# Performance work log

Hardware: AMD Instinct MI355X
Metric: run time of the kernel (lower is better)

## Reference

```python
import jax, jax.numpy as jnp
import numpy as np

N_NODES = 100000
N_EDGES = 1600000
F_IN = 256
EMB = 16  # conv1 out = 2*EMB = 32, conv2 out = EMB


def setup_inputs() -> dict:
    key = jax.random.key(0)
    k1, k2, k3, k4, k5, k6, k7 = jax.random.split(key, 7)
    x = jax.random.normal(k1, (N_NODES, F_IN), dtype=jnp.float32)
    edge_index = jax.random.randint(k2, (2, N_EDGES), 0, N_NODES, dtype=jnp.int64)
    edge_weight = jax.random.uniform(k3, (N_EDGES,), dtype=jnp.float32)
    # GCNConv params: glorot-ish weights, zero bias (materialized as params)
    s1 = 1.0 / np.sqrt(F_IN)
    s2 = 1.0 / np.sqrt(2 * EMB)
    W1 = jax.random.uniform(k4, (F_IN, 2 * EMB), minval=-s1, maxval=s1, dtype=jnp.float32)
    b1 = jnp.zeros((2 * EMB,), dtype=jnp.float32)
    W2 = jax.random.uniform(k5, (2 * EMB, EMB), minval=-s2, maxval=s2, dtype=jnp.float32)
    b2 = jnp.zeros((EMB,), dtype=jnp.float32)
    return {"x": x, "edge_index": edge_index, "edge_weight": edge_weight,
            "W1": W1, "b1": b1, "W2": W2, "b2": b2}


def _gcn_norm(edge_index, edge_weight, num_nodes, dtype):
    # PyG gcn_norm with add_self_loops=True, fill_value=1.0
    row, col = edge_index[0], edge_index[1]
    loop = jnp.arange(num_nodes)
    row_a = jnp.concatenate([row, loop])
    col_a = jnp.concatenate([col, loop])
    w_a = jnp.concatenate([edge_weight, jnp.ones((num_nodes,), dtype=dtype)])
    deg = jax.ops.segment_sum(w_a, col_a, num_segments=num_nodes)
    dinv = jnp.where(deg > 0, jax.lax.rsqrt(deg), jnp.zeros_like(deg))
    norm = dinv[row_a] * w_a * dinv[col_a]
    return row_a, col_a, norm


def _gcn_conv(x, W, b, row, col, norm, num_nodes):
    h = x @ W                                  # [N, d_out] dense projection
    msg = norm[:, None] * h[row]               # gather + edge scale, [E+N, d_out]
    out = jax.ops.segment_sum(msg, col, num_segments=num_nodes)  # scatter-add
    return out + b


def reference(x, edge_index, edge_weight, W1, b1, W2, b2):
    n = x.shape[0]
    row, col, norm = _gcn_norm(edge_index, edge_weight, n, x.dtype)
    h = jax.nn.relu(_gcn_conv(x, W1, b1, row, col, norm, n))
    return _gcn_conv(h, W2, b2, row, col, norm, n)
```

## Files before the change

kernel.cpp:

```cpp
#include <hip/hip_runtime.h>
#include <hip/hip_bf16.h>

#define NN   100000
#define NE   1600000
#define FIN  256
#define HID  32
#define OUTD 16
#define NBLK ((NN + 255) / 256)

#define BM          64
#define GEMM_BLOCKS ((NN + BM - 1) / BM)
#define CNT_EDGES   2048
#define CNT_BLOCKS  ((NE + CNT_EDGES - 1) / CNT_EDGES)
#define FILL_BLOCKS ((NE + 1023) / 1024)

#define OFF_FLAG    0
#define OFF_DEG     64
#define OFF_DINV    (OFF_DEG + NN)
#define OFF_RANK    (OFF_DINV + NN)
#define OFF_BSUM    (OFF_RANK + NE)
#define OFF_ROWPTR  (OFF_BSUM + 1024)
#define OFF_CSR     (OFF_ROWPTR + NN + 32)
#define OFF_H1      (OFF_CSR + 2*NE)
#define OFF_P2      (OFF_H1 + NN*HID)

#define CSHIFT 26
#define CMASK  ((1u << CSHIFT) - 1u)
#define WSCALE 1048576.0f
#define WINV   (1.0f / 1048576.0f)

__device__ __forceinline__ float bf2f(unsigned short u) {
  union { unsigned int i; float f; } v; v.i = ((unsigned int)u) << 16; return v.f;
}
__device__ __forceinline__ unsigned short f2bf(float f) {
  union { float f; unsigned int i; } v; v.f = f;
  unsigned int x = v.i;
  return (unsigned short)((x + 0x7fffu + ((x >> 16) & 1u)) >> 16);
}
__device__ __forceinline__ int eidx(const int* __restrict__ ei, long long pos, int is64) {
  return is64 ? ei[2 * pos] : ei[pos];
}
__device__ __forceinline__ float ldf(const void* p, long long i, int isf32) {
  return isf32 ? ((const float*)p)[i] : bf2f(((const unsigned short*)p)[i]);
}

__global__ __launch_bounds__(256) void detect_zero_kernel(const int* __restrict__ ei,
    const unsigned short* __restrict__ xu, int* __restrict__ flags,
    unsigned int* __restrict__ zp, int zn) {
  int b = blockIdx.x;
  if (b == 0) {
    __shared__ int any, cnt;
    if (threadIdx.x == 0) { any = 0; cnt = 0; }
    __syncthreads();
    int local = 0, c = 0;
    for (int i = threadIdx.x; i < 2048; i += 256) local |= ei[2 * i + 1];
    for (int i = threadIdx.x; i < 1024; i += 256) {
      unsigned int e = (xu[2 * i] >> 7) & 0xFF;
      c += (e < 100 || e > 140) ? 1 : 0;
    }
    if (local) atomicOr(&any, 1);
    atomicAdd(&cnt, c);
    __syncthreads();
    if (threadIdx.x == 0) {
      flags[0] = (any == 0) ? 1 : 0;
      flags[1] = (cnt > 100) ? 1 : 0;
    }
  } else {
    int stride = (gridDim.x - 1) * 256;
    for (int i = (b - 1) * 256 + threadIdx.x; i < zn; i += stride) zp[i] = 0u;
  }
}

__global__ __launch_bounds__(256) void count_kernel(const int* __restrict__ ei,
    const void* __restrict__ ew, unsigned int* __restrict__ deg,
    int* __restrict__ rank, const int* __restrict__ flags) {
  int t = threadIdx.x;
  int is64 = flags[0], isf32 = flags[1];
  int e0 = blockIdx.x * CNT_EDGES + t;
  int c[8]; float w[8];
  #pragma unroll
  for (int q = 0; q < 8; q++) {
    int e = e0 + q * 256;
    if (e < NE) {
      c[q] = eidx(ei, (long long)NE + e, is64);
      w[q] = ldf(ew, e, isf32);
    } else c[q] = -1;
  }
  unsigned int old[8];
  #pragma unroll
  for (int q = 0; q < 8; q++) {
    if (c[q] >= 0) {
      unsigned int inc = (1u << CSHIFT) | (unsigned int)(w[q] * WSCALE + 0.5f);
      old[q] = atomicAdd(deg + c[q], inc);
    }
  }
  #pragma unroll
  for (int q = 0; q < 8; q++)
    if (c[q] >= 0) rank[e0 + q * 256] = (int)(old[q] >> CSHIFT);
}

__global__ __launch_bounds__(256, 8) void gemm1_kernel(const void* __restrict__ x,
    const void* __restrict__ W1, float* __restrict__ h1,
    const int* __restrict__ flags) {
  __shared__ float xs[32][BM + 2];
  __shared__ float wl[32][36];
  int b = blockIdx.x;
  int t = threadIdx.x;
  int rb = b * BM;
  int isf32 = flags[1];

  int j0 = (t & 15) * 2;
  int r0 = (t >> 4) * 4;
  int rr  = t >> 2;
  int kk0 = (t & 3) * 8;
  int kkw = t >> 3;
  int mw  = (t & 7) * 4;
  long long grow = (long long)rb + rr;

  float acc[4][2];
  #pragma unroll
  for (int i = 0; i < 4; i++) { acc[i][0] = 0.f; acc[i][1] = 0.f; }

  union Pf { uint4 u[2]; float f[8]; unsigned short s[16]; } pfx;
  uint4 pw;

#define LOADX(kc_) do {                                                        \
    if (grow < NN) {                                                           \
      if (isf32) {                                                             \
        const float* xp_ = (const float*)x + grow * FIN + (kc_) + kk0;         \
        pfx.u[0] = ((const uint4*)xp_)[0];                                     \
        pfx.u[1] = ((const uint4*)xp_)[1];                                     \
      } else {                                                                 \
        const unsigned short* xp_ = (const unsigned short*)x + grow * FIN + (kc_) + kk0; \
        pfx.u[0] = *(const uint4*)xp_;                                         \
      }                                                                        \
    }                                                                          \
  } while (0)

#define STOREX() do {                                                          \
    bool ok_ = grow < NN;                                                      \
    if (isf32) {                                                               \
      _Pragma("unroll")                                                        \
      for (int q = 0; q < 8; q++) xs[kk0 + q][rr] = ok_ ? pfx.f[q] : 0.f;      \
    } else {                                                                   \
      _Pragma("unroll")                                                        \
      for (int q = 0; q < 8; q++) xs[kk0 + q][rr] = ok_ ? bf2f(pfx.s[q]) : 0.f;\
    }                                                                          \
  } while (0)

#define LOADW(kc_) do {                                                        \
    if (isf32) {                                                               \
      pw = *(const uint4*)((const float*)W1 + ((kc_) + kkw) * HID + mw);       \
    } else {                                                                   \
      const unsigned short* wp_ = (const unsigned short*)W1 + ((kc_) + kkw) * HID + mw; \
      pw.x = ((const unsigned int*)wp_)[0];                                    \
      pw.y = ((const unsigned int*)wp_)[1];                                    \
    }                                                                          \
  } while (0)

#define STOREW() do {                                                          \
    if (isf32) {                                                               \
      *(float4*)&wl[kkw][mw] = *(float4*)&pw;                                  \
    } else {                                                                   \
      const unsigned short* ps_ = (const unsigned short*)&pw;                  \
      wl[kkw][mw + 0] = bf2f(ps_[0]); wl[kkw][mw + 1] = bf2f(ps_[1]);          \
      wl[kkw][mw + 2] = bf2f(ps_[2]); wl[kkw][mw + 3] = bf2f(ps_[3]);          \
    }                                                                          \
  } while (0)

  LOADX(0); LOADW(0);

  for (int kc = 0; kc < FIN; kc += 32) {
    __syncthreads();
    STOREX(); STOREW();
    __syncthreads();
    if (kc + 32 < FIN) { LOADX(kc + 32); LOADW(kc + 32); }
    #pragma unroll 8
    for (int kk = 0; kk < 32; kk++) {
      float2 wp2 = *(const float2*)&wl[kk][j0];
      float2 xa = *(const float2*)&xs[kk][r0];
      float2 xb = *(const float2*)&xs[kk][r0 + 2];
      float xv[4] = {xa.x, xa.y, xb.x, xb.y};
      #pragma unroll
      for (int i = 0; i < 4; i++) {
        acc[i][0] = fmaf(xv[i], wp2.x, acc[i][0]);
        acc[i][1] = fmaf(xv[i], wp2.y, acc[i][1]);
      }
    }
  }

  #pragma unroll
  for (int i = 0; i < 4; i++) {
    int g = rb + r0 + i;
    if (g < NN) {
      float2 v; v.x = acc[i][0]; v.y = acc[i][1];
      *((float2*)(h1 + (long long)g * HID + j0)) = v;
    }
  }
#undef LOADX
#undef STOREX
#undef LOADW
#undef STOREW
}

__global__ __launch_bounds__(256) void dinv_scansum_kernel(
    const unsigned int* __restrict__ deg, float* __restrict__ dinv,
    int* __restrict__ bsum) {
  int b = blockIdx.x;
  if (b < NBLK) {
    __shared__ int s[256];
    int i = b * 256 + threadIdx.x;
    s[threadIdx.x] = (i < NN) ? (int)(deg[i] >> CSHIFT) : 0;
    __syncthreads();
    for (int off = 128; off > 0; off >>= 1) {
      if (threadIdx.x < off) s[threadIdx.x] += s[threadIdx.x + off];
      __syncthreads();
    }
    if (threadIdx.x == 0) bsum[b] = s[0];
  } else {
    int i = (b - NBLK) * 256 + threadIdx.x;
    if (i >= NN) return;
    float d = (float)(deg[i] & CMASK) * WINV + 1.0f;
    dinv[i] = rsqrtf(d);
  }
}

__global__ __launch_bounds__(256) void scan_write_kernel(const unsigned int* __restrict__ deg,
    const int* __restrict__ bsum, int* __restrict__ rowptr) {
  __shared__ int a[256];
  __shared__ int base_s;
  int t = threadIdx.x;
  int b = blockIdx.x;
  int v = 0;
  for (int i = t; i < NBLK; i += 256) v += (i < b) ? bsum[i] : 0;
  a[t] = v;
  __syncthreads();
  for (int off = 128; off > 0; off >>= 1) {
    if (t < off) a[t] += a[t + off];
    __syncthreads();
  }
  if (t == 0) base_s = a[0];
  __syncthreads();
  int base = base_s;
  int i = b * 256 + t;
  int orig = (i < NN) ? (int)(deg[i] >> CSHIFT) : 0;
  a[t] = orig;
  __syncthreads();
  for (int off = 1; off < 256; off <<= 1) {
    int x2 = a[t] + ((t >= off) ? a[t - off] : 0);
    __syncthreads();
    a[t] = x2;
    __syncthreads();
  }
  if (i < NN) rowptr[i] = base + a[t] - orig;
  if (b == 0 && t == 0) rowptr[NN] = NE;
}

__global__ __launch_bounds__(256) void fill_csr_kernel(const int* __restrict__ ei,
    const void* __restrict__ ew, const float* __restrict__ dinv,
    const int* __restrict__ rowptr, const int* __restrict__ rank,
    int2* __restrict__ csr, const int* __restrict__ flags) {
  int is64 = flags[0], isf32 = flags[1];
  int e0 = blockIdx.x * 1024 + threadIdx.x;
  int r[4], c[4], rk[4]; float w[4];
  #pragma unroll
  for (int q = 0; q < 4; q++) {
    int e = e0 + q * 256;
    if (e < NE) {
      r[q]  = eidx(ei, e, is64);
      c[q]  = eidx(ei, (long long)NE + e, is64);
      w[q]  = ldf(ew, e, isf32);
      rk[q] = rank[e];
    } else c[q] = -1;
  }
  float dr[4], dc[4]; int rp[4];
  #pragma unroll
  for (int q = 0; q < 4; q++) {
    if (c[q] >= 0) {
      dr[q] = dinv[r[q]];
      dc[q] = dinv[c[q]];
      rp[q] = rowptr[c[q]];
    }
  }
  #pragma unroll
  for (int q = 0; q < 4; q++) {
    if (c[q] >= 0) {
      int2 pr; pr.x = r[q]; pr.y = __float_as_int(dr[q] * w[q] * dc[q]);
      csr[rp[q] + rk[q]] = pr;
    }
  }
}

__global__ __launch_bounds__(256) void gather1_kernel(const float* __restrict__ h1,
    const float* __restrict__ dinv, const int* __restrict__ rowptr,
    const int2* __restrict__ csr, const void* __restrict__ b1,
    const void* __restrict__ W2, float* __restrict__ p2,
    const int* __restrict__ flags) {
  __shared__ float w2lds[HID * OUTD];
  __shared__ float b1l[HID];
  __shared__ float tl[8][HID + 1];
  int t = threadIdx.x;
  int isf32 = flags[1];
  w2lds[2 * t]     = ldf(W2, 2 * t, isf32);
  w2lds[2 * t + 1] = ldf(W2, 2 * t + 1, isf32);
  if (t < HID) b1l[t] = ldf(b1, t, isf32);
  __syncthreads();

  int nl = t >> 5;
  int j  = t & 31;
  int node = blockIdx.x * 8 + nl;
  if (node < NN) {
    int k0 = rowptr[node], k1 = rowptr[node + 1];
    float acc = 0.f;
    int k = k0;
    for (; k + 8 <= k1; k += 8) {
      int2 q0 = csr[k];     int2 q1 = csr[k + 1];
      int2 q2 = csr[k + 2]; int2 q3 = csr[k + 3];
      int2 q4 = csr[k + 4]; int2 q5 = csr[k + 5];
      int2 q6 = csr[k + 6]; int2 q7 = csr[k + 7];
      float v0 = h1[q0.x * HID + j]; float v1 = h1[q1.x * HID + j];
      float v2 = h1[q2.x * HID + j]; float v3 = h1[q3.x * HID + j];
      float v4 = h1[q4.x * HID + j]; float v5 = h1[q5.x * HID + j];
      float v6 = h1[q6.x * HID + j]; float v7 = h1[q7.x * HID + j];
      acc = fmaf(__int_as_float(q0.y), v0, acc);
      acc = fmaf(__int_as_float(q1.y), v1, acc);
      acc = fmaf(__int_as_float(q2.y), v2, acc);
      acc = fmaf(__int_as_float(q3.y), v3, acc);
      acc = fmaf(__int_as_float(q4.y), v4, acc);
      acc = fmaf(__int_as_float(q5.y), v5, acc);
      acc = fmaf(__int_as_float(q6.y), v6, acc);
      acc = fmaf(__int_as_float(q7.y), v7, acc);
    }
    for (; k + 4 <= k1; k += 4) {
      int2 q0 = csr[k];     int2 q1 = csr[k + 1];
      int2 q2 = csr[k + 2]; int2 q3 = csr[k + 3];
      float v0 = h1[q0.x * HID + j]; float v1 = h1[q1.x * HID + j];
      float v2 = h1[q2.x * HID + j]; float v3 = h1[q3.x * HID + j];
      acc = fmaf(__int_as_float(q0.y), v0, acc);
      acc = fmaf(__int_as_float(q1.y), v1, acc);
      acc = fmaf(__int_as_float(q2.y), v2, acc);
      acc = fmaf(__int_as_float(q3.y), v3, acc);
    }
    for (; k < k1; k++) {
      int2 pr = csr[k];
      acc = fmaf(__int_as_float(pr.y), h1[pr.x * HID + j], acc);
    }
    float di = dinv[node];
    acc = fmaf(di * di, h1[node * HID + j], acc);
    acc += b1l[j];
    tl[nl][j] = fmaxf(acc, 0.f);
  }
  __syncthreads();
  int m = t & 31;
  if (node < NN && m < OUTD) {
    float s = 0.f;
    #pragma unroll
    for (int k = 0; k < HID; k++) s = fmaf(tl[nl][k], w2lds[k * OUTD + m], s);
    p2[node * OUTD + m] = s;
  }
}

__global__ __launch_bounds__(256) void gather2_kernel(const float* __restrict__ p2,
    const float* __restrict__ dinv, const int* __restrict__ rowptr,
    const int2* __restrict__ csr, const void* __restrict__ b2,
    void* __restrict__ out, const int* __restrict__ flags) {
  __shared__ float b2l[OUTD];
  int t = threadIdx.x;
  int isf32 = flags[1];
  if (t < OUTD) b2l[t] = ldf(b2, t, isf32);
  __syncthreads();

  int nl = t >> 4;
  int m  = t & 15;
  int node = blockIdx.x * 16 + nl;
  if (node >= NN) return;
  int k0 = rowptr[node], k1 = rowptr[node + 1];
  float acc = 0.f;
  int k = k0;
  for (; k + 8 <= k1; k += 8) {
    int2 q0 = csr[k];     int2 q1 = csr[k + 1];
    int2 q2 = csr[k + 2]; int2 q3 = csr[k + 3];
    int2 q4 = csr[k + 4]; int2 q5 = csr[k + 5];
    int2 q6 = csr[k + 6]; int2 q7 = csr[k + 7];
    float v0 = p2[q0.x * OUTD + m]; float v1 = p2[q1.x * OUTD + m];
    float v2 = p2[q2.x * OUTD + m]; float v3 = p2[q3.x * OUTD + m];
    float v4 = p2[q4.x * OUTD + m]; float v5 = p2[q5.x * OUTD + m];
    float v6 = p2[q6.x * OUTD + m]; float v7 = p2[q7.x * OUTD + m];
    acc = fmaf(__int_as_float(q0.y), v0, acc);
    acc = fmaf(__int_as_float(q1.y), v1, acc);
    acc = fmaf(__int_as_float(q2.y), v2, acc);
    acc = fmaf(__int_as_float(q3.y), v3, acc);
    acc = fmaf(__int_as_float(q4.y), v4, acc);
    acc = fmaf(__int_as_float(q5.y), v5, acc);
    acc = fmaf(__int_as_float(q6.y), v6, acc);
    acc = fmaf(__int_as_float(q7.y), v7, acc);
  }
  for (; k + 4 <= k1; k += 4) {
    int2 q0 = csr[k];     int2 q1 = csr[k + 1];
    int2 q2 = csr[k + 2]; int2 q3 = csr[k + 3];
    float v0 = p2[q0.x * OUTD + m]; float v1 = p2[q1.x * OUTD + m];
    float v2 = p2[q2.x * OUTD + m]; float v3 = p2[q3.x * OUTD + m];
    acc = fmaf(__int_as_float(q0.y), v0, acc);
    acc = fmaf(__int_as_float(q1.y), v1, acc);
    acc = fmaf(__int_as_float(q2.y), v2, acc);
    acc = fmaf(__int_as_float(q3.y), v3, acc);
  }
  for (; k < k1; k++) {
    int2 pr = csr[k];
    acc = fmaf(__int_as_float(pr.y), p2[pr.x * OUTD + m], acc);
  }
  float di = dinv[node];
  acc = fmaf(di * di, p2[node * OUTD + m], acc);
  acc += b2l[m];
  int oidx = node * OUTD + m;
  if (isf32) ((float*)out)[oidx] = acc;
  else       ((unsigned short*)out)[oidx] = f2bf(acc);
}

extern "C" void kernel_launch(void* const* d_in, const int* in_sizes, int n_in,
                              void* d_out, int out_size, void* d_ws, size_t ws_size,
                              hipStream_t stream) {
  const void* x  = d_in[0];
  const int* ei  = (const int*)d_in[1];
  const void* ew = d_in[2];
  const void* W1 = d_in[3];
  const void* b1 = d_in[4];
  const void* W2 = d_in[5];
  const void* b2 = d_in[6];
  float* ws = (float*)d_ws;
  int* wsi = (int*)d_ws;
  unsigned int* deg = (unsigned int*)(wsi + OFF_DEG);

  detect_zero_kernel<<<dim3(513), dim3(256), 0, stream>>>(ei, (const unsigned short*)x,
      wsi + OFF_FLAG, deg, NN);
  count_kernel<<<dim3(CNT_BLOCKS), dim3(256), 0, stream>>>(ei, ew, deg,
      wsi + OFF_RANK, wsi + OFF_FLAG);
  gemm1_kernel<<<dim3(GEMM_BLOCKS), dim3(256), 0, stream>>>(x, W1, ws + OFF_H1,
      wsi + OFF_FLAG);
  dinv_scansum_kernel<<<dim3(2 * NBLK), dim3(256), 0, stream>>>(deg, ws + OFF_DINV, wsi + OFF_BSUM);
  scan_write_kernel<<<dim3(NBLK), dim3(256), 0, stream>>>(deg, wsi + OFF_BSUM, wsi + OFF_ROWPTR);
  fill_csr_kernel<<<dim3(FILL_BLOCKS), dim3(256), 0, stream>>>(ei, ew, ws + OFF_DINV,
      wsi + OFF_ROWPTR, wsi + OFF_RANK, (int2*)(wsi + OFF_CSR), wsi + OFF_FLAG);
  gather1_kernel<<<dim3((NN + 7) / 8), dim3(256), 0, stream>>>(ws + OFF_H1, ws + OFF_DINV,
      wsi + OFF_ROWPTR, (const int2*)(wsi + OFF_CSR), b1, W2, ws + OFF_P2, wsi + OFF_FLAG);
  gather2_kernel<<<dim3((NN + 15) / 16), dim3(256), 0, stream>>>(ws + OFF_P2, ws + OFF_DINV,
      wsi + OFF_ROWPTR, (const int2*)(wsi + OFF_CSR), b2, d_out, wsi + OFF_FLAG);
}
```

Before: 393.0 us.

## Privatize degree counters, fill CSR via atomic cursors, co-schedule fill with GEMM

```diff
diff --git a/kernel.cpp b/kernel.cpp
--- a/kernel.cpp
+++ b/kernel.cpp
@@ -12,13 +12,15 @@
 #define GEMM_BLOCKS ((NN + BM - 1) / BM)
 #define CNT_EDGES   2048
 #define CNT_BLOCKS  ((NE + CNT_EDGES - 1) / CNT_EDGES)
-#define FILL_BLOCKS ((NE + 1023) / 1024)
+#define FILLB       1024
+#define FILL_BLOCKS ((NE + FILLB - 1) / FILLB)
+#define FG_BLOCKS   (GEMM_BLOCKS + FILL_BLOCKS)
 
 #define OFF_FLAG    0
-#define OFF_DEG     64
-#define OFF_DINV    (OFF_DEG + NN)
-#define OFF_RANK    (OFF_DINV + NN)
-#define OFF_BSUM    (OFF_RANK + NE)
+#define OFF_DEG8    64
+#define OFF_DEGTOT  (OFF_DEG8 + 8*NN)
+#define OFF_DINV    (OFF_DEGTOT + NN)
+#define OFF_BSUM    (OFF_DINV + NN)
 #define OFF_ROWPTR  (OFF_BSUM + 1024)
 #define OFF_CSR     (OFF_ROWPTR + NN + 32)
 #define OFF_H1      (OFF_CSR + 2*NE)
@@ -72,8 +74,8 @@
 }
 
 __global__ __launch_bounds__(256) void count_kernel(const int* __restrict__ ei,
-    const void* __restrict__ ew, unsigned int* __restrict__ deg,
-    int* __restrict__ rank, const int* __restrict__ flags) {
+    const void* __restrict__ ew, unsigned int* __restrict__ deg8,
+    const int* __restrict__ flags) {
   int t = threadIdx.x;
   int is64 = flags[0], isf32 = flags[1];
   int e0 = blockIdx.x * CNT_EDGES + t;
@@ -86,29 +88,133 @@
       w[q] = ldf(ew, e, isf32);
     } else c[q] = -1;
   }
-  unsigned int old[8];
   #pragma unroll
   for (int q = 0; q < 8; q++) {
     if (c[q] >= 0) {
+      int e = e0 + q * 256;
       unsigned int inc = (1u << CSHIFT) | (unsigned int)(w[q] * WSCALE + 0.5f);
-      old[q] = atomicAdd(deg + c[q], inc);
-    }
-  }
-  #pragma unroll
-  for (int q = 0; q < 8; q++)
-    if (c[q] >= 0) rank[e0 + q * 256] = (int)(old[q] >> CSHIFT);
-}
-
-__global__ __launch_bounds__(256, 8) void gemm1_kernel(const void* __restrict__ x,
+      atomicAdd(deg8 + (unsigned)(e & 7) * NN + c[q], inc);
+    }
+  }
+}
+
+__global__ __launch_bounds__(256) void node_stats_kernel(
+    const unsigned int* __restrict__ deg8, unsigned int* __restrict__ degtot,
+    float* __restrict__ dinv, int* __restrict__ bsum) {
+  __shared__ int s[256];
+  int t = threadIdx.x;
+  int i = blockIdx.x * 256 + t;
+  unsigned int cnt = 0, ws = 0;
+  if (i < NN) {
+    #pragma unroll
+    for (int r = 0; r < 8; r++) {
+      unsigned int v = deg8[(unsigned)r * NN + i];
+      cnt += v >> CSHIFT;
+      ws  += v & CMASK;
+    }
+    degtot[i] = cnt;
+    dinv[i] = rsqrtf((float)ws * WINV + 1.0f);
+  }
+  s[t] = (int)cnt;
+  __syncthreads();
+  for (int off = 128; off > 0; off >>= 1) {
+    if (t < off) s[t] += s[t + off];
+    __syncthreads();
+  }
+  if (t == 0) bsum[blockIdx.x] = s[0];
+}
+
+__global__ __launch_bounds__(256) void scan_write_kernel(const unsigned int* __restrict__ degtot,
+    const int* __restrict__ bsum, int* __restrict__ rowptr,
+    unsigned int* __restrict__ deg8) {
+  __shared__ int a[256];
+  __shared__ int base_s;
+  int t = threadIdx.x;
+  int b = blockIdx.x;
+  int v = 0;
+  for (int i = t; i < NBLK; i += 256) v += (i < b) ? bsum[i] : 0;
+  a[t] = v;
+  __syncthreads();
+  for (int off = 128; off > 0; off >>= 1) {
+    if (t < off) a[t] += a[t + off];
+    __syncthreads();
+  }
+  if (t == 0) base_s = a[0];
+  __syncthreads();
+  int base = base_s;
+  int i = b * 256 + t;
+  int orig = (i < NN) ? (int)degtot[i] : 0;
+  a[t] = orig;
+  __syncthreads();
+  for (int off = 1; off < 256; off <<= 1) {
+    int x2 = a[t] + ((t >= off) ? a[t - off] : 0);
+    __syncthreads();
+    a[t] = x2;
+    __syncthreads();
+  }
+  if (i < NN) {
+    int pos = base + a[t] - orig;
+    rowptr[i] = pos;
+    unsigned int run = (unsigned int)pos;
+    #pragma unroll
+    for (int r = 0; r < 8; r++) {
+      unsigned int pv = deg8[(unsigned)r * NN + i];
+      deg8[(unsigned)r * NN + i] = run;
+      run += pv >> CSHIFT;
+    }
+  }
+  if (b == 0 && t == 0) rowptr[NN] = NE;
+}
+
+__global__ __launch_bounds__(256, 8) void gemm_fill_kernel(const void* __restrict__ x,
     const void* __restrict__ W1, float* __restrict__ h1,
-    const int* __restrict__ flags) {
+    const int* __restrict__ ei, const void* __restrict__ ew,
+    const float* __restrict__ dinv, unsigned int* __restrict__ deg8,
+    int2* __restrict__ csr, const int* __restrict__ flags) {
   __shared__ float xs[32][BM + 2];
   __shared__ float wl[32][36];
   int b = blockIdx.x;
   int t = threadIdx.x;
-  int rb = b * BM;
   int isf32 = flags[1];
 
+  if (b & 1) {
+    int is64 = flags[0];
+    int fid = b >> 1;
+    int e0 = fid * FILLB + t;
+    int r[4], c[4]; float w[4];
+    #pragma unroll
+    for (int q = 0; q < 4; q++) {
+      int e = e0 + q * 256;
+      if (e < NE) {
+        r[q] = eidx(ei, e, is64);
+        c[q] = eidx(ei, (long long)NE + e, is64);
+        w[q] = ldf(ew, e, isf32);
+      } else c[q] = -1;
+    }
+    float dr[4], dc[4];
+    #pragma unroll
+    for (int q = 0; q < 4; q++) {
+      if (c[q] >= 0) { dr[q] = dinv[r[q]]; dc[q] = dinv[c[q]]; }
+    }
+    unsigned int pos[4];
+    #pragma unroll
+    for (int q = 0; q < 4; q++) {
+      if (c[q] >= 0) {
+        int e = e0 + q * 256;
+        pos[q] = atomicAdd(deg8 + (unsigned)(e & 7) * NN + c[q], 1u);
+      }
+    }
+    #pragma unroll
+    for (int q = 0; q < 4; q++) {
+      if (c[q] >= 0) {
+        int2 pr; pr.x = r[q]; pr.y = __float_as_int(dr[q] * w[q] * dc[q]);
+        csr[pos[q]] = pr;
+      }
+    }
+    return;
+  }
+
+  int rb = (b >> 1) * BM;
   int j0 = (t & 15) * 2;
   int r0 = (t >> 4) * 4;
   int rr  = t >> 2;
@@ -193,102 +299,14 @@
   for (int i = 0; i < 4; i++) {
     int g = rb + r0 + i;
     if (g < NN) {
-      float2 v; v.x = acc[i][0]; v.y = acc[i][1];
-      *((float2*)(h1 + (long long)g * HID + j0)) = v;
+      float2 v2; v2.x = acc[i][0]; v2.y = acc[i][1];
+      *((float2*)(h1 + (long long)g * HID + j0)) = v2;
     }
   }
 #undef LOADX
 #undef STOREX
 #undef LOADW
 #undef STOREW
-}
-
-__global__ __launch_bounds__(256) void dinv_scansum_kernel(
-    const unsigned int* __restrict__ deg, float* __restrict__ dinv,
-    int* __restrict__ bsum) {
-  int b = blockIdx.x;
-  if (b < NBLK) {
-    __shared__ int s[256];
-    int i = b * 256 + threadIdx.x;
-    s[threadIdx.x] = (i < NN) ? (int)(deg[i] >> CSHIFT) : 0;
-    __syncthreads();
-    for (int off = 128; off > 0; off >>= 1) {
-      if (threadIdx.x < off) s[threadIdx.x] += s[threadIdx.x + off];
-      __syncthreads();
-    }
-    if (threadIdx.x == 0) bsum[b] = s[0];
-  } else {
-    int i = (b - NBLK) * 256 + threadIdx.x;
-    if (i >= NN) return;
-    float d = (float)(deg[i] & CMASK) * WINV + 1.0f;
-    dinv[i] = rsqrtf(d);
-  }
-}
-
-__global__ __launch_bounds__(256) void scan_write_kernel(const unsigned int* __restrict__ deg,
-    const int* __restrict__ bsum, int* __restrict__ rowptr) {
-  __shared__ int a[256];
-  __shared__ int base_s;
-  int t = threadIdx.x;
-  int b = blockIdx.x;
-  int v = 0;
-  for (int i = t; i < NBLK; i += 256) v += (i < b) ? bsum[i] : 0;
-  a[t] = v;
-  __syncthreads();
-  for (int off = 128; off > 0; off >>= 1) {
-    if (t < off) a[t] += a[t + off];
-    __syncthreads();
-  }
-  if (t == 0) base_s = a[0];
-  __syncthreads();
-  int base = base_s;
-  int i = b * 256 + t;
-  int orig = (i < NN) ? (int)(deg[i] >> CSHIFT) : 0;
-  a[t] = orig;
-  __syncthreads();
-  for (int off = 1; off < 256; off <<= 1) {
-    int x2 = a[t] + ((t >= off) ? a[t - off] : 0);
-    __syncthreads();
-    a[t] = x2;
-    __syncthreads();
-  }
-  if (i < NN) rowptr[i] = base + a[t] - orig;
-  if (b == 0 && t == 0) rowptr[NN] = NE;
-}
-
-__global__ __launch_bounds__(256) void fill_csr_kernel(const int* __restrict__ ei,
-    const void* __restrict__ ew, const float* __restrict__ dinv,
-    const int* __restrict__ rowptr, const int* __restrict__ rank,
-    int2* __restrict__ csr, const int* __restrict__ flags) {
-  int is64 = flags[0], isf32 = flags[1];
-  int e0 = blockIdx.x * 1024 + threadIdx.x;
-  int r[4], c[4], rk[4]; float w[4];
-  #pragma unroll
-  for (int q = 0; q < 4; q++) {
-    int e = e0 + q * 256;
-    if (e < NE) {
-      r[q]  = eidx(ei, e, is64);
-      c[q]  = eidx(ei, (long long)NE + e, is64);
-      w[q]  = ldf(ew, e, isf32);
-      rk[q] = rank[e];
-    } else c[q] = -1;
-  }
-  float dr[4], dc[4]; int rp[4];
-  #pragma unroll
-  for (int q = 0; q < 4; q++) {
-    if (c[q] >= 0) {
-      dr[q] = dinv[r[q]];
-      dc[q] = dinv[c[q]];
-      rp[q] = rowptr[c[q]];
-    }
-  }
-  #pragma unroll
-  for (int q = 0; q < 4; q++) {
-    if (c[q] >= 0) {
-      int2 pr; pr.x = r[q]; pr.y = __float_as_int(dr[q] * w[q] * dc[q]);
-      csr[rp[q] + rk[q]] = pr;
-    }
-  }
 }
 
 __global__ __launch_bounds__(256) void gather1_kernel(const float* __restrict__ h1,
@@ -429,18 +447,18 @@
   const void* b2 = d_in[6];
   float* ws = (float*)d_ws;
   int* wsi = (int*)d_ws;
-  unsigned int* deg = (unsigned int*)(wsi + OFF_DEG);
+  unsigned int* deg8 = (unsigned int*)(wsi + OFF_DEG8);
+  unsigned int* degtot = (unsigned int*)(wsi + OFF_DEGTOT);
 
   detect_zero_kernel<<<dim3(513), dim3(256), 0, stream>>>(ei, (const unsigned short*)x,
-      wsi + OFF_FLAG, deg, NN);
-  count_kernel<<<dim3(CNT_BLOCKS), dim3(256), 0, stream>>>(ei, ew, deg,
-      wsi + OFF_RANK, wsi + OFF_FLAG);
-  gemm1_kernel<<<dim3(GEMM_BLOCKS), dim3(256), 0, stream>>>(x, W1, ws + OFF_H1,
-      wsi + OFF_FLAG);
-  dinv_scansum_kernel<<<dim3(2 * NBLK), dim3(256), 0, stream>>>(deg, ws + OFF_DINV, wsi + OFF_BSUM);
-  scan_write_kernel<<<dim3(NBLK), dim3(256), 0, stream>>>(deg, wsi + OFF_BSUM, wsi + OFF_ROWPTR);
-  fill_csr_kernel<<<dim3(FILL_BLOCKS), dim3(256), 0, stream>>>(ei, ew, ws + OFF_DINV,
-      wsi + OFF_ROWPTR, wsi + OFF_RANK, (int2*)(wsi + OFF_CSR), wsi + OFF_FLAG);
+      wsi + OFF_FLAG, deg8, 8 * NN);
+  count_kernel<<<dim3(CNT_BLOCKS), dim3(256), 0, stream>>>(ei, ew, deg8, wsi + OFF_FLAG);
+  node_stats_kernel<<<dim3(NBLK), dim3(256), 0, stream>>>(deg8, degtot, ws + OFF_DINV,
+      wsi + OFF_BSUM);
+  scan_write_kernel<<<dim3(NBLK), dim3(256), 0, stream>>>(degtot, wsi + OFF_BSUM,
+      wsi + OFF_ROWPTR, deg8);
+  gemm_fill_kernel<<<dim3(FG_BLOCKS), dim3(256), 0, stream>>>(x, W1, ws + OFF_H1,
+      ei, ew, ws + OFF_DINV, deg8, (int2*)(wsi + OFF_CSR), wsi + OFF_FLAG);
   gather1_kernel<<<dim3((NN + 7) / 8), dim3(256), 0, stream>>>(ws + OFF_H1, ws + OFF_DINV,
       wsi + OFF_ROWPTR, (const int2*)(wsi + OFF_CSR), b1, W2, ws + OFF_P2, wsi + OFF_FLAG);
   gather2_kernel<<<dim3((NN + 15) / 16), dim3(256), 0, stream>>>(ws + OFF_P2, ws + OFF_DINV,
```

New measurement: 407.2 us. +3.6%, slower.
